# Kernel tuning notes

Hardware: AMD Instinct MI355X
Metric: run time of the kernel (lower is better)

## Reference

```python
import jax, jax.numpy as jnp
import numpy as np

B, S, D, H = 2, 2048, 1024, 16
DK = D // H

def setup_inputs() -> dict:
    key = jax.random.key(0)
    ks = jax.random.split(key, 9)
    def lin(k, fan_in):
        bound = 1.0 / np.sqrt(fan_in)
        kw, kb = jax.random.split(k)
        w = jax.random.uniform(kw, (D, D), jnp.float32, -bound, bound)
        b = jax.random.uniform(kb, (D,), jnp.float32, -bound, bound)
        return w, b
    Wq_w, Wq_b = lin(ks[0], D)
    Wk_w, Wk_b = lin(ks[1], D)
    Wv_w, Wv_b = lin(ks[2], D)
    Wo_w, Wo_b = lin(ks[3], D)
    x = jax.random.normal(ks[4], (B, S, D), jnp.float32)
    mask = jnp.ones((B, 1, 1, S), jnp.int32)
    return {"x": x, "mask": mask,
            "Wq_w": Wq_w, "Wq_b": Wq_b, "Wk_w": Wk_w, "Wk_b": Wk_b,
            "Wv_w": Wv_w, "Wv_b": Wv_b, "Wo_w": Wo_w, "Wo_b": Wo_b}

def reference(x, mask, Wq_w, Wq_b, Wk_w, Wk_b, Wv_w, Wv_b, Wo_w, Wo_b):
    b, s, d = x.shape
    def split_heads(t):  # [B,S,D] -> [B,H,S,DK]
        return t.reshape(b, s, H, DK).transpose(0, 2, 1, 3)
    Q = split_heads(x @ Wq_w.T + Wq_b)
    K = split_heads(x @ Wk_w.T + Wk_b)
    V = split_heads(x @ Wv_w.T + Wv_b)
    scale = 1.0 / jnp.sqrt(jnp.float32(DK))
    scores = jnp.einsum('bhqd,bhkd->bhqk', Q, K) * scale  # [B,H,S,S]
    scores = jnp.where(mask == 0, jnp.float32(-1e9), scores)
    attn = jax.nn.softmax(scores, axis=-1)
    context = jnp.einsum('bhqk,bhkd->bhqd', attn, V)  # [B,H,S,DK]
    context = context.transpose(0, 2, 1, 3).reshape(b, s, d)
    return context @ Wo_w.T + Wo_b
```

## Files before the change

### kernel.cpp

```cpp
#include <hip/hip_runtime.h>
#include <hip/hip_bf16.h>


#define DEV __device__ __forceinline__

typedef __bf16 bf16_t;
typedef __bf16 bf16x4 __attribute__((ext_vector_type(4)));
typedef __bf16 bf16x8 __attribute__((ext_vector_type(8)));
typedef float f32x4 __attribute__((ext_vector_type(4)));

constexpr int Ss = 2048, Dd = 1024, Hh = 16, DKk = 64;
constexpr float QSCALE = 0.125f * 1.4426950408889634f;

DEV void gload_lds16(const void* g, void* l) {
  __builtin_amdgcn_global_load_lds(
      (__attribute__((address_space(1))) void*)(g),
      (__attribute__((address_space(3))) void*)(l), 16, 0, 0);
}

DEV bf16_t f2b(float v) { return (bf16_t)v; }

DEV float fast_exp2(float x) {
#if __has_builtin(__builtin_amdgcn_exp2f)
  return __builtin_amdgcn_exp2f(x);
#else
  return exp2f(x);
#endif
}

DEV void cvt16_core(const float* src, bf16_t* dst) {
  const float4* s4 = (const float4*)src;
  float4 a = s4[0], b = s4[1], c = s4[2], d = s4[3];
  bf16x8 lo = {f2b(a.x), f2b(a.y), f2b(a.z), f2b(a.w), f2b(b.x), f2b(b.y), f2b(b.z), f2b(b.w)};
  bf16x8 hi = {f2b(c.x), f2b(c.y), f2b(c.z), f2b(c.w), f2b(d.x), f2b(d.y), f2b(d.z), f2b(d.w)};
  *(bf16x8*)dst = lo;
  *(bf16x8*)(dst + 8) = hi;
}

__global__ __launch_bounds__(256) void cvt16(const float* __restrict__ x,
                                             bf16_t* __restrict__ xb) {
  size_t i = ((size_t)blockIdx.x * 256 + threadIdx.x) * 16;
  cvt16_core(x + i, xb + i);
}

__global__ __launch_bounds__(256) void cvt_all(
    const float* __restrict__ x,
    const float* __restrict__ wq, const float* __restrict__ wk,
    const float* __restrict__ wv, const float* __restrict__ wo,
    bf16_t* __restrict__ xb, bf16_t* __restrict__ Wb) {
  size_t i = ((size_t)blockIdx.x * 256 + threadIdx.x) * 16;
  const size_t XN = (size_t)4 << 20;
  if (i < XN) {
    cvt16_core(x + i, xb + i);
  } else {
    size_t j = i - XN;
    int z = (int)(j >> 20);
    size_t o = j & (((size_t)1 << 20) - 1);
    const float* s = (z == 0) ? wq : ((z == 1) ? wk : ((z == 2) ? wv : wo));
    cvt16_core(s + o, Wb + j);
  }
}

template <bool WB16>
__global__ __launch_bounds__(256) void gemm_qkv(
    const bf16_t* __restrict__ A,
    const float* __restrict__ W0, const float* __restrict__ W1, const float* __restrict__ W2,
    const bf16_t* __restrict__ Wb,
    const float* __restrict__ b0, const float* __restrict__ b1, const float* __restrict__ b2,
    bf16_t* __restrict__ o0, bf16_t* __restrict__ o1, bf16_t* __restrict__ o2) {
  const int z = blockIdx.z;
  const float* Wf = (z == 0) ? W0 : ((z == 1) ? W1 : W2);
  const bf16_t* Wbf = Wb + (size_t)z * (1u << 20);
  const float* bias = (z == 0) ? b0 : ((z == 1) ? b1 : b2);
  bf16_t* out = (z == 0) ? o0 : ((z == 1) ? o1 : o2);
  const float oscale = (z == 0) ? QSCALE : 1.0f;

  __shared__ __align__(16) bf16_t As[128 * 32];
  __shared__ __align__(16) bf16_t Ws[128 * 32];

  const int tid = threadIdx.x;
  const int lane = tid & 63, w = tid >> 6;
  const int quad = lane >> 4, c = lane & 15;
  const int wm = w >> 1, wn = w & 1;
  const int m0 = blockIdx.y * 128, n0 = blockIdx.x * 128;
  const int trow = tid >> 1, tcol = (tid & 1) * 16;
  const int srow = lane >> 2, scol = (lane & 3) * 8;

  const f32x4 vzero = {0.f, 0.f, 0.f, 0.f};
  f32x4 acc[4][4];
  for (int i = 0; i < 4; i++)
    for (int j = 0; j < 4; j++) acc[i][j] = vzero;

  for (int k0 = 0; k0 < 1024; k0 += 32) {
    for (int r = 0; r < 2; r++) {
      int row = r * 64 + w * 16;
      gload_lds16(&A[(size_t)(m0 + row + srow) * 1024 + k0 + scol], &As[row * 32]);
      if (WB16)
        gload_lds16(&Wbf[(size_t)(n0 + row + srow) * 1024 + k0 + scol], &Ws[row * 32]);
    }
    if (!WB16)
      cvt16_core(&Wf[(size_t)(n0 + trow) * 1024 + k0 + tcol], &Ws[trow * 32 + tcol]);
    __syncthreads();

    bf16x8 af[4], bfr[4];
    for (int i = 0; i < 4; i++)
      af[i] = *(const bf16x8*)&As[(wm * 64 + i * 16 + c) * 32 + quad * 8];
    for (int j = 0; j < 4; j++)
      bfr[j] = *(const bf16x8*)&Ws[(wn * 64 + j * 16 + c) * 32 + quad * 8];
    for (int i = 0; i < 4; i++)
      for (int j = 0; j < 4; j++)
        acc[i][j] = __builtin_amdgcn_mfma_f32_16x16x32_bf16(af[i], bfr[j], acc[i][j], 0, 0, 0);
    __syncthreads();
  }

  for (int j = 0; j < 4; j++) {
    int n = n0 + wn * 64 + j * 16 + c;
    float bv = bias[n];
    for (int i = 0; i < 4; i++) {
      int mbase = m0 + wm * 64 + i * 16 + quad * 4;
      int b_ = mbase >> 11, s_ = mbase & 2047;
      int h_ = n >> 6, dk_ = n & 63;
      if (z < 2) {
        for (int r = 0; r < 4; r++)
          out[((size_t)(b_ * Hh + h_) * Ss + (s_ + r)) * DKk + dk_] =
              f2b((acc[i][j][r] + bv) * oscale);
      } else {
        bf16x4 pk;
        for (int r = 0; r < 4; r++) pk[r] = f2b(acc[i][j][r] + bv);
        *(bf16x4*)&out[((size_t)(b_ * Hh + h_) * DKk + dk_) * Ss + s_] = pk;
      }
    }
  }
}

__global__ __launch_bounds__(128) void attn_fwd(
    const bf16_t* __restrict__ Q, const bf16_t* __restrict__ K,
    const bf16_t* __restrict__ Vt, const int* __restrict__ mask,
    bf16_t* __restrict__ ctx) {
  __shared__ __align__(16) bf16_t Ks[2][64 * 64];
  __shared__ __align__(16) bf16_t Vts[2][64 * 64];

  const int tid = threadIdx.x, lane = tid & 63, w = tid >> 6;
  const int quad = lane >> 4, c = lane & 15;
  const int c7 = c & 7;
  const int bh = blockIdx.y, b_ = bh >> 4, h_ = bh & 15;
  const int q0 = blockIdx.x * 64 + w * 32;
  const size_t head = (size_t)bh * Ss * DKk;
  const int* maskb = mask + b_ * Ss;

  const int sr = lane >> 3;
  const int gc = (lane & 7) ^ sr;

  for (int r = 0; r < 4; r++) {
    int row = w * 32 + r * 8;
    gload_lds16(&K[head + (size_t)(row + sr) * 64 + gc * 8], &Ks[0][row * 64]);
    gload_lds16(&Vt[head + (size_t)(row + sr) * Ss + gc * 8], &Vts[0][row * 64]);
  }

  bf16x8 qf[2][2];
  for (int mi = 0; mi < 2; mi++)
    for (int ks = 0; ks < 2; ks++)
      qf[mi][ks] = *(const bf16x8*)&Q[head + (size_t)(q0 + mi * 16 + c) * DKk + ks * 32 + quad * 8];

  int4 mk4[4];
  for (int ni = 0; ni < 4; ni++) mk4[ni] = *(const int4*)&maskb[ni * 16 + quad * 4];

  const bf16_t oneb = f2b(1.0f), zb = f2b(0.0f);
  const bf16x8 ones = {oneb, oneb, oneb, oneb, zb, zb, zb, zb};

  const f32x4 vzero = {0.f, 0.f, 0.f, 0.f};
  f32x4 o[2][4];
  for (int mi = 0; mi < 2; mi++)
    for (int t = 0; t < 4; t++) o[mi][t] = vzero;
  f32x4 ol[2] = {vzero, vzero};

  constexpr int NT = Ss / 64;
  for (int kt = 0; kt < NT; kt++) {
    const int cur = kt & 1;
    __syncthreads();

    if (kt + 1 < NT) {
      int nxt = cur ^ 1;
      for (int r = 0; r < 4; r++) {
        int row = w * 32 + r * 8;
        gload_lds16(&K[head + (size_t)((kt + 1) * 64 + row + sr) * 64 + gc * 8],
                    &Ks[nxt][row * 64]);
        gload_lds16(&Vt[head + (size_t)(row + sr) * Ss + (kt + 1) * 64 + gc * 8],
                    &Vts[nxt][row * 64]);
      }
    }
    int4 mk4n[4];
    if (kt + 1 < NT)
      for (int ni = 0; ni < 4; ni++)
        mk4n[ni] = *(const int4*)&maskb[(kt + 1) * 64 + ni * 16 + quad * 4];

    f32x4 sc[2][4];
    for (int mi = 0; mi < 2; mi++)
      for (int ni = 0; ni < 4; ni++) sc[mi][ni] = vzero;
    for (int ks = 0; ks < 2; ks++) {
      int pc = ((ks * 4 + quad) ^ c7) * 8;
      for (int ni = 0; ni < 4; ni++) {
        bf16x8 kf = *(const bf16x8*)&Ks[cur][(ni * 16 + c) * 64 + pc];
        sc[0][ni] = __builtin_amdgcn_mfma_f32_16x16x32_bf16(kf, qf[0][ks], sc[0][ni], 0, 0, 0);
        sc[1][ni] = __builtin_amdgcn_mfma_f32_16x16x32_bf16(kf, qf[1][ks], sc[1][ni], 0, 0, 0);
      }
    }

    f32x4 mb[4];
    for (int ni = 0; ni < 4; ni++) {
      mb[ni][0] = mk4[ni].x ? 0.f : -1e9f;
      mb[ni][1] = mk4[ni].y ? 0.f : -1e9f;
      mb[ni][2] = mk4[ni].z ? 0.f : -1e9f;
      mb[ni][3] = mk4[ni].w ? 0.f : -1e9f;
    }

    for (int ni = 0; ni < 4; ni++) {
      bf16x8 a0, a1;
      for (int r = 0; r < 4; r++) {
        a0[r] = f2b(fast_exp2(sc[0][ni][r] + mb[ni][r]));
        a1[r] = f2b(fast_exp2(sc[1][ni][r] + mb[ni][r]));
        a0[4 + r] = zb;
        a1[4 + r] = zb;
      }
      const int vcol = (((ni * 2 + (quad >> 1)) ^ c7) * 8) + (quad & 1) * 4;
      for (int t = 0; t < 4; t++) {
        bf16x4 v4 = *(const bf16x4*)&Vts[cur][(t * 16 + c) * 64 + vcol];
        bf16x8 vf = {v4[0], v4[1], v4[2], v4[3], zb, zb, zb, zb};
        o[0][t] = __builtin_amdgcn_mfma_f32_16x16x32_bf16(a0, vf, o[0][t], 0, 0, 0);
        o[1][t] = __builtin_amdgcn_mfma_f32_16x16x32_bf16(a1, vf, o[1][t], 0, 0, 0);
      }
      ol[0] = __builtin_amdgcn_mfma_f32_16x16x32_bf16(a0, ones, ol[0], 0, 0, 0);
      ol[1] = __builtin_amdgcn_mfma_f32_16x16x32_bf16(a1, ones, ol[1], 0, 0, 0);
    }

    for (int ni = 0; ni < 4; ni++) mk4[ni] = mk4n[ni];
  }

  for (int mi = 0; mi < 2; mi++) {
    float inv[4];
    for (int r = 0; r < 4; r++) inv[r] = 1.0f / ol[mi][r];
    for (int t = 0; t < 4; t++)
      for (int r = 0; r < 4; r++) {
        int s_ = q0 + mi * 16 + quad * 4 + r;
        ctx[((size_t)(b_ * Ss + s_)) * Dd + h_ * 64 + t * 16 + c] =
            f2b(o[mi][t][r] * inv[r]);
      }
  }
}

template <bool WB16>
__global__ __launch_bounds__(256) void gemm_out(
    const bf16_t* __restrict__ A, const float* __restrict__ Wf,
    const bf16_t* __restrict__ Wb, const float* __restrict__ bias,
    float* __restrict__ out) {
  __shared__ __align__(16) bf16_t As[64 * 32];
  __shared__ __align__(16) bf16_t Ws[128 * 32];

  const int tid = threadIdx.x;
  const int lane = tid & 63, w = tid >> 6;
  const int quad = lane >> 4, c = lane & 15;
  const int wm = w >> 1, wn = w & 1;
  const int m0 = blockIdx.y * 64, n0 = blockIdx.x * 128;
  const int trow = tid >> 1, tcol = (tid & 1) * 16;
  const int srow = lane >> 2, scol = (lane & 3) * 8;

  const f32x4 vzero = {0.f, 0.f, 0.f, 0.f};
  f32x4 acc[2][4];
  for (int i = 0; i < 2; i++)
    for (int j = 0; j < 4; j++) acc[i][j] = vzero;

  for (int k0 = 0; k0 < 1024; k0 += 32) {
    gload_lds16(&A[(size_t)(m0 + w * 16 + srow) * 1024 + k0 + scol], &As[(w * 16) * 32]);
    if (WB16) {
      for (int r = 0; r < 2; r++) {
        int row = r * 64 + w * 16;
        gload_lds16(&Wb[(size_t)(n0 + row + srow) * 1024 + k0 + scol], &Ws[row * 32]);
      }
    } else {
      cvt16_core(&Wf[(size_t)(n0 + trow) * 1024 + k0 + tcol], &Ws[trow * 32 + tcol]);
    }
    __syncthreads();

    bf16x8 af[2], bfr[4];
    for (int i = 0; i < 2; i++)
      af[i] = *(const bf16x8*)&As[(wm * 32 + i * 16 + c) * 32 + quad * 8];
    for (int j = 0; j < 4; j++)
      bfr[j] = *(const bf16x8*)&Ws[(wn * 64 + j * 16 + c) * 32 + quad * 8];
    for (int i = 0; i < 2; i++)
      for (int j = 0; j < 4; j++)
        acc[i][j] = __builtin_amdgcn_mfma_f32_16x16x32_bf16(af[i], bfr[j], acc[i][j], 0, 0, 0);
    __syncthreads();
  }

  for (int j = 0; j < 4; j++) {
    int n = n0 + wn * 64 + j * 16 + c;
    float bv = bias[n];
    for (int i = 0; i < 2; i++) {
      int mbase = m0 + wm * 32 + i * 16 + quad * 4;
      for (int r = 0; r < 4; r++)
        out[(size_t)(mbase + r) * 1024 + n] = acc[i][j][r] + bv;
    }
  }
}

extern "C" void kernel_launch(void* const* d_in, const int* in_sizes, int n_in,
                              void* d_out, int out_size, void* d_ws, size_t ws_size,
                              hipStream_t stream) {
  const float* x  = (const float*)d_in[0];
  const int* mask = (const int*)d_in[1];
  const float* Wq = (const float*)d_in[2];
  const float* bq = (const float*)d_in[3];
  const float* Wk = (const float*)d_in[4];
  const float* bk = (const float*)d_in[5];
  const float* Wv = (const float*)d_in[6];
  const float* bv = (const float*)d_in[7];
  const float* Wo = (const float*)d_in[8];
  const float* bo = (const float*)d_in[9];
  float* out = (float*)d_out;

  bf16_t* ws = (bf16_t*)d_ws;
  const size_t QKV_ELEMS = (size_t)2 * Hh * Ss * DKk;
  bf16_t* xb  = ws;
  bf16_t* Qb  = ws + QKV_ELEMS;
  bf16_t* Kb  = ws + 2 * QKV_ELEMS;
  bf16_t* Vt  = ws + 3 * QKV_ELEMS;
  bf16_t* Wb  = ws + 4 * QKV_ELEMS;
  bf16_t* ctx = xb;

  const bool wb16 = ws_size >= (size_t)40 * 1024 * 1024;

  if (wb16) {
    cvt_all<<<dim3(2048), 256, 0, stream>>>(x, Wq, Wk, Wv, Wo, xb, Wb);
    gemm_qkv<true><<<dim3(8, 32, 3), 256, 0, stream>>>(
        xb, Wq, Wk, Wv, Wb, bq, bk, bv, Qb, Kb, Vt);
  } else {
    cvt16<<<dim3(1024), 256, 0, stream>>>(x, xb);
    gemm_qkv<false><<<dim3(8, 32, 3), 256, 0, stream>>>(
        xb, Wq, Wk, Wv, ws , bq, bk, bv, Qb, Kb, Vt);
  }
  attn_fwd<<<dim3(Ss / 64, 2 * Hh), 128, 0, stream>>>(Qb, Kb, Vt, mask, ctx);
  if (wb16)
    gemm_out<true><<<dim3(8, 64), 256, 0, stream>>>(ctx, Wo, Wb + 3 * (1u << 20), bo, out);
  else
    gemm_out<false><<<dim3(8, 64), 256, 0, stream>>>(ctx, Wo, ws , bo, out);
}
```

Before: 222.2 us.

## Restructure attention into single-wave blocks with register K/V and LDS-staged P

The attention kernel now runs one wave per block over 32 queries, with launch bounds allowing two blocks per SIMD. K and V^T fragments are loaded straight from global memory into registers each tile, replacing the double-buffered LDS staging and block barriers. Softmax probabilities are written to a swizzled LDS tile and read back as full 32-wide K fragments, so the PV and row-sum MFMAs no longer carry half-zero operands and fewer of them are issued. The cost is losing K/V sharing across waves and the async prefetch, which adds redundant global/L2 traffic and exposes load latency.

```diff
diff --git a/kernel.cpp b/kernel.cpp
--- a/kernel.cpp
+++ b/kernel.cpp
@@ -133,40 +133,27 @@
   }
 }
 
-__global__ __launch_bounds__(128) void attn_fwd(
+__global__ __launch_bounds__(64, 2) void attn_fwd(
     const bf16_t* __restrict__ Q, const bf16_t* __restrict__ K,
     const bf16_t* __restrict__ Vt, const int* __restrict__ mask,
     bf16_t* __restrict__ ctx) {
-  __shared__ __align__(16) bf16_t Ks[2][64 * 64];
-  __shared__ __align__(16) bf16_t Vts[2][64 * 64];
-
-  const int tid = threadIdx.x, lane = tid & 63, w = tid >> 6;
+  __shared__ __align__(16) bf16_t Ps[32 * 64];
+
+  const int lane = threadIdx.x & 63;
   const int quad = lane >> 4, c = lane & 15;
   const int c7 = c & 7;
   const int bh = blockIdx.y, b_ = bh >> 4, h_ = bh & 15;
-  const int q0 = blockIdx.x * 64 + w * 32;
+  const int q0 = blockIdx.x * 32;
   const size_t head = (size_t)bh * Ss * DKk;
   const int* maskb = mask + b_ * Ss;
-
-  const int sr = lane >> 3;
-  const int gc = (lane & 7) ^ sr;
-
-  for (int r = 0; r < 4; r++) {
-    int row = w * 32 + r * 8;
-    gload_lds16(&K[head + (size_t)(row + sr) * 64 + gc * 8], &Ks[0][row * 64]);
-    gload_lds16(&Vt[head + (size_t)(row + sr) * Ss + gc * 8], &Vts[0][row * 64]);
-  }
 
   bf16x8 qf[2][2];
   for (int mi = 0; mi < 2; mi++)
     for (int ks = 0; ks < 2; ks++)
       qf[mi][ks] = *(const bf16x8*)&Q[head + (size_t)(q0 + mi * 16 + c) * DKk + ks * 32 + quad * 8];
 
-  int4 mk4[4];
-  for (int ni = 0; ni < 4; ni++) mk4[ni] = *(const int4*)&maskb[ni * 16 + quad * 4];
-
-  const bf16_t oneb = f2b(1.0f), zb = f2b(0.0f);
-  const bf16x8 ones = {oneb, oneb, oneb, oneb, zb, zb, zb, zb};
+  const bf16_t oneb = f2b(1.0f);
+  const bf16x8 ones = {oneb, oneb, oneb, oneb, oneb, oneb, oneb, oneb};
 
   const f32x4 vzero = {0.f, 0.f, 0.f, 0.f};
   f32x4 o[2][4];
@@ -176,64 +163,48 @@
 
   constexpr int NT = Ss / 64;
   for (int kt = 0; kt < NT; kt++) {
-    const int cur = kt & 1;
-    __syncthreads();
-
-    if (kt + 1 < NT) {
-      int nxt = cur ^ 1;
-      for (int r = 0; r < 4; r++) {
-        int row = w * 32 + r * 8;
-        gload_lds16(&K[head + (size_t)((kt + 1) * 64 + row + sr) * 64 + gc * 8],
-                    &Ks[nxt][row * 64]);
-        gload_lds16(&Vt[head + (size_t)(row + sr) * Ss + (kt + 1) * 64 + gc * 8],
-                    &Vts[nxt][row * 64]);
-      }
-    }
-    int4 mk4n[4];
-    if (kt + 1 < NT)
+    bf16x8 kf[2][4], vf[2][4];
+    const bf16_t* Kt = K + head + (size_t)kt * 64 * DKk;
+    for (int ks = 0; ks < 2; ks++)
       for (int ni = 0; ni < 4; ni++)
-        mk4n[ni] = *(const int4*)&maskb[(kt + 1) * 64 + ni * 16 + quad * 4];
+        kf[ks][ni] = *(const bf16x8*)&Kt[(ni * 16 + c) * DKk + ks * 32 + quad * 8];
+    for (int ks = 0; ks < 2; ks++)
+      for (int t = 0; t < 4; t++)
+        vf[ks][t] = *(const bf16x8*)&Vt[head + (size_t)(t * 16 + c) * Ss + kt * 64 + ks * 32 + quad * 8];
+    int mk[4];
+    for (int ni = 0; ni < 4; ni++) mk[ni] = maskb[kt * 64 + ni * 16 + c];
 
     f32x4 sc[2][4];
     for (int mi = 0; mi < 2; mi++)
       for (int ni = 0; ni < 4; ni++) sc[mi][ni] = vzero;
+    for (int ks = 0; ks < 2; ks++)
+      for (int ni = 0; ni < 4; ni++) {
+        sc[0][ni] = __builtin_amdgcn_mfma_f32_16x16x32_bf16(qf[0][ks], kf[ks][ni], sc[0][ni], 0, 0, 0);
+        sc[1][ni] = __builtin_amdgcn_mfma_f32_16x16x32_bf16(qf[1][ks], kf[ks][ni], sc[1][ni], 0, 0, 0);
+      }
+
+    for (int mi = 0; mi < 2; mi++)
+      for (int ni = 0; ni < 4; ni++) {
+        float mb = mk[ni] ? 0.f : -1e9f;
+        for (int r = 0; r < 4; r++) {
+          float p = fast_exp2(sc[mi][ni][r] + mb);
+          int ql = mi * 16 + quad * 4 + r;
+          int chunk = (ni * 2 + (c >> 3)) ^ (ql & 7);
+          Ps[ql * 64 + chunk * 8 + c7] = f2b(p);
+        }
+      }
+
     for (int ks = 0; ks < 2; ks++) {
       int pc = ((ks * 4 + quad) ^ c7) * 8;
-      for (int ni = 0; ni < 4; ni++) {
-        bf16x8 kf = *(const bf16x8*)&Ks[cur][(ni * 16 + c) * 64 + pc];
-        sc[0][ni] = __builtin_amdgcn_mfma_f32_16x16x32_bf16(kf, qf[0][ks], sc[0][ni], 0, 0, 0);
-        sc[1][ni] = __builtin_amdgcn_mfma_f32_16x16x32_bf16(kf, qf[1][ks], sc[1][ni], 0, 0, 0);
-      }
-    }
-
-    f32x4 mb[4];
-    for (int ni = 0; ni < 4; ni++) {
-      mb[ni][0] = mk4[ni].x ? 0.f : -1e9f;
-      mb[ni][1] = mk4[ni].y ? 0.f : -1e9f;
-      mb[ni][2] = mk4[ni].z ? 0.f : -1e9f;
-      mb[ni][3] = mk4[ni].w ? 0.f : -1e9f;
-    }
-
-    for (int ni = 0; ni < 4; ni++) {
-      bf16x8 a0, a1;
-      for (int r = 0; r < 4; r++) {
-        a0[r] = f2b(fast_exp2(sc[0][ni][r] + mb[ni][r]));
-        a1[r] = f2b(fast_exp2(sc[1][ni][r] + mb[ni][r]));
-        a0[4 + r] = zb;
-        a1[4 + r] = zb;
-      }
-      const int vcol = (((ni * 2 + (quad >> 1)) ^ c7) * 8) + (quad & 1) * 4;
+      bf16x8 pf0 = *(const bf16x8*)&Ps[c * 64 + pc];
+      bf16x8 pf1 = *(const bf16x8*)&Ps[(16 + c) * 64 + pc];
       for (int t = 0; t < 4; t++) {
-        bf16x4 v4 = *(const bf16x4*)&Vts[cur][(t * 16 + c) * 64 + vcol];
-        bf16x8 vf = {v4[0], v4[1], v4[2], v4[3], zb, zb, zb, zb};
-        o[0][t] = __builtin_amdgcn_mfma_f32_16x16x32_bf16(a0, vf, o[0][t], 0, 0, 0);
-        o[1][t] = __builtin_amdgcn_mfma_f32_16x16x32_bf16(a1, vf, o[1][t], 0, 0, 0);
-      }
-      ol[0] = __builtin_amdgcn_mfma_f32_16x16x32_bf16(a0, ones, ol[0], 0, 0, 0);
-      ol[1] = __builtin_amdgcn_mfma_f32_16x16x32_bf16(a1, ones, ol[1], 0, 0, 0);
-    }
-
-    for (int ni = 0; ni < 4; ni++) mk4[ni] = mk4n[ni];
+        o[0][t] = __builtin_amdgcn_mfma_f32_16x16x32_bf16(pf0, vf[ks][t], o[0][t], 0, 0, 0);
+        o[1][t] = __builtin_amdgcn_mfma_f32_16x16x32_bf16(pf1, vf[ks][t], o[1][t], 0, 0, 0);
+      }
+      ol[0] = __builtin_amdgcn_mfma_f32_16x16x32_bf16(pf0, ones, ol[0], 0, 0, 0);
+      ol[1] = __builtin_amdgcn_mfma_f32_16x16x32_bf16(pf1, ones, ol[1], 0, 0, 0);
+    }
   }
 
   for (int mi = 0; mi < 2; mi++) {
@@ -338,7 +309,7 @@
     gemm_qkv<false><<<dim3(8, 32, 3), 256, 0, stream>>>(
         xb, Wq, Wk, Wv, ws , bq, bk, bv, Qb, Kb, Vt);
   }
-  attn_fwd<<<dim3(Ss / 64, 2 * Hh), 128, 0, stream>>>(Qb, Kb, Vt, mask, ctx);
+  attn_fwd<<<dim3(Ss / 32, 2 * Hh), 64, 0, stream>>>(Qb, Kb, Vt, mask, ctx);
   if (wb16)
     gemm_out<true><<<dim3(8, 64), 256, 0, stream>>>(ctx, Wo, Wb + 3 * (1u << 20), bo, out);
   else
```

Result: slower. 279.5 us (+25.8%).
